# Performance work log

Hardware: AMD Instinct MI355X
Metric: run time of the kernel (lower is better)

Reference implementation:

```python
import jax, jax.numpy as jnp
import numpy as np
import math

EPS = 1e-5
NUM_HEADS = 8

def _ln(x, g, b):
    m = x.mean(-1, keepdims=True)
    v = ((x - m) ** 2).mean(-1, keepdims=True)
    return (x - m) / jnp.sqrt(v + EPS) * g + b

def _swish(x):
    return x * jax.nn.sigmoid(x)

def _rope(x):
    # lucidrains RotaryEmbedding.rotate_queries_or_keys: rotates along axis -2,
    # interleaved pair convention, base 10000.
    n, d = x.shape[-2], x.shape[-1]
    inv = 1.0 / (10000.0 ** (jnp.arange(0, d, 2, dtype=jnp.float32) / d))
    freqs = jnp.arange(n, dtype=jnp.float32)[:, None] * inv[None, :]  # (n, d/2)
    cos = jnp.repeat(jnp.cos(freqs), 2, axis=-1)  # (n, d)
    sin = jnp.repeat(jnp.sin(freqs), 2, axis=-1)
    x1, x2 = x[..., 0::2], x[..., 1::2]
    rot = jnp.stack([-x2, x1], axis=-1).reshape(x.shape)
    return x * cos + rot * sin

def _ffn(x, w1, b1, w2, b2):
    # FeedForwardModule: x + 0.5 * (Linear -> Swish -> Linear)
    return x + 0.5 * (_swish(x @ w1 + b1) @ w2 + b2)

def _mhsa(x, g, b, wq, bq, wk, bk, wv, bv, wo, bo):
    B, T, D = x.shape
    dh = D // NUM_HEADS
    y = _ln(x, g, b)
    q = (y @ wq + bq).reshape(B, T, NUM_HEADS, dh)                         # (b,t,h,d)
    k = (y @ wk + bk).reshape(B, T, NUM_HEADS, dh).transpose(0, 2, 1, 3)   # (b,h,t,d)
    v = (y @ wv + bv).reshape(B, T, NUM_HEADS, dh).transpose(0, 2, 1, 3)
    # Faithful to source: query is NOT permuted before rotary, so RoPE acts on
    # axis -2 which is heads for q and time for k (matches torch code exactly).
    q = _rope(q).transpose(0, 2, 1, 3)                                     # (b,h,t,d)
    k = _rope(k)
    score = jnp.einsum('bhtd,bhsd->bhts', q, k) / math.sqrt(D)             # /sqrt(d_model)
    attn = jax.nn.softmax(score, axis=-1)
    ctx = jnp.einsum('bhts,bhsd->bhtd', attn, v).transpose(0, 2, 1, 3).reshape(B, T, D)
    return x + ctx @ wo + bo

def _conv_module(x, g, b, pw1_w, pw1_b, dw_w, dw_b, bn_g, bn_b, pw2_w, pw2_b):
    C = dw_w.shape[-1]  # 2*dim
    y = _ln(x, g, b)
    y = jnp.einsum('btd,ed->bte', y, pw1_w) + pw1_b            # pointwise conv (b,t,4*dim)
    a, gate = y[..., :C], y[..., C:]
    y = a * jax.nn.sigmoid(gate)                                # GLU over channel dim
    y = jax.lax.conv_general_dilated(
        y, dw_w, window_strides=(1,), padding='SAME',
        dimension_numbers=('NWC', 'WIO', 'NWC'), feature_group_count=C) + dw_b
    m = y.mean(axis=(0, 1))                                     # BatchNorm1d, training stats
    v = ((y - m) ** 2).mean(axis=(0, 1))
    y = (y - m) / jnp.sqrt(v + EPS) * bn_g + bn_b
    y = _swish(y)
    y = jnp.einsum('btc,dc->btd', y, pw2_w) + pw2_b             # pointwise conv back to dim
    return x + y

def setup_inputs():
    key = jax.random.key(0)
    B, T, D, K = 8, 1024, 512, 31
    HID = 2 * D
    C = 2 * D
    ks = jax.random.split(key, 16)
    rn = lambda k, shp: jax.random.normal(k, shp, jnp.float32) * 0.02
    zeros = lambda n: jnp.zeros((n,), jnp.float32)
    ones = lambda n: jnp.ones((n,), jnp.float32)
    return dict(
        x=jax.random.normal(ks[0], (B, T, D), jnp.float32),
        ffn1_w1=rn(ks[1], (D, HID)), ffn1_b1=zeros(HID),
        ffn1_w2=rn(ks[2], (HID, D)), ffn1_b2=zeros(D),
        ln_attn_g=ones(D), ln_attn_b=zeros(D),
        wq=rn(ks[3], (D, D)), bq=zeros(D),
        wk=rn(ks[4], (D, D)), bk=zeros(D),
        wv=rn(ks[5], (D, D)), bv=zeros(D),
        wo=rn(ks[6], (D, D)), bo=zeros(D),
        conv_ln_g=ones(D), conv_ln_b=zeros(D),
        pw1_w=rn(ks[7], (2 * C, D)), pw1_b=zeros(2 * C),
        dw_w=rn(ks[8], (K, 1, C)), dw_b=zeros(C),
        bn_g=ones(C), bn_b=zeros(C),
        pw2_w=rn(ks[9], (D, C)), pw2_b=zeros(D),
        ffn2_w1=rn(ks[10], (D, HID)), ffn2_b1=zeros(HID),
        ffn2_w2=rn(ks[11], (HID, D)), ffn2_b2=zeros(D),
        ln_out_g=ones(D), ln_out_b=zeros(D),
    )

def reference(x, ffn1_w1, ffn1_b1, ffn1_w2, ffn1_b2, ln_attn_g, ln_attn_b,
              wq, bq, wk, bk, wv, bv, wo, bo,
              conv_ln_g, conv_ln_b, pw1_w, pw1_b, dw_w, dw_b, bn_g, bn_b, pw2_w, pw2_b,
              ffn2_w1, ffn2_b1, ffn2_w2, ffn2_b2, ln_out_g, ln_out_b):
    y = _ffn(x, ffn1_w1, ffn1_b1, ffn1_w2, ffn1_b2)
    y = _mhsa(y, ln_attn_g, ln_attn_b, wq, bq, wk, bk, wv, bv, wo, bo)
    y = _conv_module(y, conv_ln_g, conv_ln_b, pw1_w, pw1_b, dw_w, dw_b, bn_g, bn_b, pw2_w, pw2_b)
    y = _ffn(y, ffn2_w1, ffn2_b1, ffn2_w2, ffn2_b2)
    return _ln(y, ln_out_g, ln_out_b)
```

## Files before the change

kernel.cpp:

```cpp
#include <hip/hip_runtime.h>
#include <hip/hip_bf16.h>


#define M_ROWS 8192

using bf16x8 = __attribute__((ext_vector_type(8))) short;
using f32x4  = __attribute__((ext_vector_type(4))) float;
using s8v    = __attribute__((ext_vector_type(8))) short;
using s4v    = __attribute__((ext_vector_type(4))) short;

__device__ __forceinline__ float sigmoid_(float v) { return 1.f / (1.f + expf(-v)); }

__device__ __forceinline__ float bf2f(short s) {
  return __uint_as_float(((unsigned)(unsigned short)s) << 16);
}
__device__ __forceinline__ short f2bf(float f) {
  __hip_bfloat16 h = __float2bfloat16(f);
  return *reinterpret_cast<short*>(&h);
}

__device__ __forceinline__ void gl16(const void* g, void* l) {
  __builtin_amdgcn_global_load_lds((const __attribute__((address_space(1))) void*)g,
                                   (__attribute__((address_space(3))) void*)l, 16, 0, 0);
}

template <int BM, int BN, int BK, int EPI>
__global__ __launch_bounds__(256) void mgemm(
    const short* __restrict__ A, const short* __restrict__ Bt,
    const float* __restrict__ bias, const float* __restrict__ res,
    const short* __restrict__ resb, short* __restrict__ outb, int M, int N, int K) {
  constexpr int WR = BM / 64;
  constexpr int WC = 4 / WR;
  constexpr int NF = BN / (16 * WC);
  constexpr int KH = BK / 32;
  constexpr int APASS = (BM * BK) / 2048;
  constexpr int BPASS = (BN * BK) / 2048;
  constexpr int RPP = 2048 / BK;
  constexpr int LPS = APASS + BPASS;
  __shared__ __align__(16) short As[2][BM * BK];
  __shared__ __align__(16) short Bs[2][BN * BK];
  __shared__ __align__(16) short vstg[EPI == 4 ? 64 * 132 : 1];
  const int tid = threadIdx.x;
  const int lane = tid & 63, wid = tid >> 6;
  const int wr = wid / WC, wc = wid % WC;
  const int nbx = gridDim.x;
  const int nwg = nbx * gridDim.y;
  int id = blockIdx.y * nbx + blockIdx.x;
  id = (id & 7) * (nwg >> 3) + (id >> 3);
  const int bm = (id / nbx) * BM;
  const int bn = (id % nbx) * BN;
  f32x4 acc[4][NF];
#pragma unroll
  for (int m = 0; m < 4; ++m)
#pragma unroll
    for (int n = 0; n < NF; ++n) acc[m][n] = (f32x4){0.f, 0.f, 0.f, 0.f};
  const short* Ablk = A + (size_t)bm * K;
  const short* Bblk = Bt + (size_t)bn * K;
  const int jl = tid & (BK / 8 - 1);
  const int r0 = tid / (BK / 8);
  const int ks = ((BK == 64) ? (jl ^ (r0 & 7)) : jl) << 3;
#define STAGE(buf, k0)                                                                 \
  do {                                                                                 \
    _Pragma("unroll")                                                                  \
    for (int p = 0; p < APASS; ++p)                                                    \
      gl16(Ablk + (size_t)(r0 + p * RPP) * K + (k0) + ks,                              \
           (char*)As[buf] + p * 4096 + wid * 1024);                                    \
    _Pragma("unroll")                                                                  \
    for (int p = 0; p < BPASS; ++p)                                                    \
      gl16(Bblk + (size_t)(r0 + p * RPP) * K + (k0) + ks,                              \
           (char*)Bs[buf] + p * 4096 + wid * 1024);                                    \
  } while (0)

  STAGE(0, 0);
  STAGE(1, BK);
  const int NS = K / BK;
  const int fr = lane & 15, fg = lane >> 4;
  const int arow = wr * 64 + fr;
  const int brow = wc * (BN / WC) + fr;
  for (int i = 0; i < NS; ++i) {
    if (i + 1 < NS) {
      if constexpr (LPS == 4)      asm volatile("s_waitcnt vmcnt(4)" ::: "memory");
      else if constexpr (LPS == 3) asm volatile("s_waitcnt vmcnt(3)" ::: "memory");
      else                         asm volatile("s_waitcnt vmcnt(2)" ::: "memory");
    } else {
      asm volatile("s_waitcnt vmcnt(0)" ::: "memory");
    }
    __builtin_amdgcn_s_barrier();
    asm volatile("" ::: "memory");
    const int cur = i & 1;
    bf16x8 af[KH][4], bfr[KH][NF];
#pragma unroll
    for (int kk = 0; kk < KH; ++kk) {
      const int cx = (BK == 64) ? (((((kk << 2) + fg)) ^ (fr & 7)) << 3)
                                : ((fg << 3) + kk * 32);
#pragma unroll
      for (int m = 0; m < 4; ++m)
        af[kk][m] = *reinterpret_cast<const bf16x8*>(&As[cur][(arow + m * 16) * BK + cx]);
#pragma unroll
      for (int n = 0; n < NF; ++n)
        bfr[kk][n] = *reinterpret_cast<const bf16x8*>(&Bs[cur][(brow + n * 16) * BK + cx]);
    }
    asm volatile("s_waitcnt lgkmcnt(0)" ::: "memory");
    __builtin_amdgcn_s_barrier();
    if ((i + 2) * BK < K) STAGE(cur, (i + 2) * BK);
#pragma unroll
    for (int kk = 0; kk < KH; ++kk)
#pragma unroll
      for (int m = 0; m < 4; ++m)
#pragma unroll
        for (int n = 0; n < NF; ++n)
          acc[m][n] = __builtin_amdgcn_mfma_f32_16x16x32_bf16(af[kk][m], bfr[kk][n],
                                                              acc[m][n], 0, 0, 0);
  }
#undef STAGE
  const int orow0 = bm + wr * 64 + ((lane >> 4) << 2);
  const int ocol0 = bn + wc * (BN / WC) + fr;

  if constexpr (EPI == 4) {
    const int sel = bn >> 9;
    const float2* tbl = (const float2*)res;
    if (sel == 2) {
      const int b_ = bm >> 10, t0v = bm & 1023;
      const int hb = (bn & 511) >> 6;
#pragma unroll
      for (int pass = 0; pass < 2; ++pass) {
        __syncthreads();
        if (wc == pass) {
#pragma unroll
          for (int m = 0; m < 4; ++m) {
            const int rl = wr * 64 + ((lane >> 4) << 2) + m * 16;
#pragma unroll
            for (int n = 0; n < NF; ++n) {
              const int dl = fr + n * 16;
              const float bv = bias[bn + wc * 64 + dl];
#pragma unroll
              for (int r = 0; r < 4; ++r)
                vstg[dl * 132 + rl + r] = f2bf(acc[m][n][r] + bv);
            }
          }
        }
        __syncthreads();
#pragma unroll
        for (int it = 0; it < 4; ++it) {
          const int c = tid + (it << 8);
          const int d = c >> 4, t8 = (c & 15) << 3;
          const s8v val = *reinterpret_cast<const s8v*>(&vstg[d * 132 + t8]);
          *reinterpret_cast<s8v*>(
              &outb[(size_t)8388608 + (((size_t)((b_ << 3) + hb + pass)) << 16) +
                    ((size_t)d << 10) + t0v + t8]) = val;
        }
      }
    } else {
      const float qsc = (sel == 0) ? 0.04419417382415922f : 1.f;
#pragma unroll
      for (int n = 0; n < NF; ++n) {
        const int col = ocol0 + n * 16;
        const int h = (col >> 6) & 7, d = col & 63;
        const int p = d >> 1;
        const float bv = bias[col];
#pragma unroll
        for (int m = 0; m < 4; ++m) {
#pragma unroll
          for (int r = 0; r < 4; ++r) {
            const int row = orow0 + m * 16 + r;
            const int b_ = row >> 10, t_ = row & 1023;
            const int pos = (sel == 0) ? h : t_;
            const float2 cs = tbl[pos * 32 + p];
            float vv = acc[m][n][r] + bv;
            const float pv = __shfl_xor(vv, 1);
            float o = ((lane & 1) == 0) ? (vv * cs.x - pv * cs.y) : (vv * cs.x + pv * cs.y);
            outb[(size_t)sel * 4194304 + (((size_t)((b_ << 3) + h)) << 16) + ((size_t)t_ << 6) + d] =
                f2bf(o * qsc);
          }
        }
      }
    }
  } else if constexpr (EPI == 6) {
    const int j = bn >> 7;
#pragma unroll
    for (int m = 0; m < 4; ++m) {
#pragma unroll
      for (int np = 0; np < NF / 2; ++np) {
        const int gc = (j << 6) + ((wc * 2 + np) << 4) + fr;
        const float ba = bias[gc];
        const float bg = bias[1024 + gc];
#pragma unroll
        for (int r = 0; r < 4; ++r) {
          const int row = orow0 + m * 16 + r;
          const float a = acc[m][2 * np][r] + ba;
          const float g = acc[m][2 * np + 1][r] + bg;
          outb[(size_t)row * 1024 + gc] = f2bf(a * sigmoid_(g));
        }
      }
    }
  } else {
#pragma unroll
    for (int m = 0; m < 4; ++m) {
#pragma unroll
      for (int n = 0; n < NF; ++n) {
        const int col = ocol0 + n * 16;
        const float bv = bias[col];
#pragma unroll
        for (int r = 0; r < 4; ++r) {
          const int row = orow0 + m * 16 + r;
          float v = acc[m][n][r] + bv;
          if constexpr (EPI == 1) {
            v = v * sigmoid_(v);
          } else if constexpr (EPI == 2) {
            v += bf2f(resb[(size_t)row * N + col]);
          } else if constexpr (EPI == 3) {
            v = bf2f(resb[(size_t)row * N + col]) + 0.5f * v;
          }
          outb[(size_t)row * N + col] = f2bf(v);
        }
      }
    }
  }
}

__device__ __forceinline__ void dev_cast8(const float* in, short* out, int i) {
  const float4 a = *reinterpret_cast<const float4*>(&in[(size_t)i * 8]);
  const float4 b = *reinterpret_cast<const float4*>(&in[(size_t)i * 8 + 4]);
  s8v o = { f2bf(a.x), f2bf(a.y), f2bf(a.z), f2bf(a.w),
            f2bf(b.x), f2bf(b.y), f2bf(b.z), f2bf(b.w) };
  *reinterpret_cast<s8v*>(&out[(size_t)i * 8]) = o;
}

__global__ __launch_bounds__(256) void prep_kernel(
    const float* __restrict__ x, short* __restrict__ xb,
    const float* __restrict__ f1w1, short* __restrict__ wf1w1,
    const float* __restrict__ f1w2, short* __restrict__ wf1w2,
    const float* __restrict__ wq, const float* __restrict__ wk,
    const float* __restrict__ wv, short* __restrict__ wqkv,
    const float* __restrict__ wo, short* __restrict__ wwo,
    const float* __restrict__ pw1, short* __restrict__ wpw1,
    const float* __restrict__ pw2, short* __restrict__ wpw2,
    const float* __restrict__ f2w1, short* __restrict__ wf2w1,
    const float* __restrict__ f2w2, short* __restrict__ wf2w2,
    const float* __restrict__ bq, const float* __restrict__ bk,
    const float* __restrict__ bv, float* __restrict__ bqkv,
    float* __restrict__ rtbl) {
  __shared__ float t[32][33];
  const int blk = blockIdx.x, tid = threadIdx.x;
  const float* tin = nullptr;
  short* tout = nullptr;
  int tK = 0, tN = 0, tr = 0, tnbx = 0;
  if (blk < 2048) {
    dev_cast8(x, xb, blk * 256 + tid);
    return;
  } else if (blk < 2560) { tin = f1w1; tout = wf1w1; tK = 512; tN = 1024; tr = blk - 2048; tnbx = 32; }
  else if (blk < 3072)   { tin = f1w2; tout = wf1w2; tK = 1024; tN = 512; tr = blk - 2560; tnbx = 16; }
  else if (blk < 3328)   { tin = wq; tout = wqkv; tK = 512; tN = 512; tr = blk - 3072; tnbx = 16; }
  else if (blk < 3584)   { tin = wk; tout = wqkv + 512 * 512; tK = 512; tN = 512; tr = blk - 3328; tnbx = 16; }
  else if (blk < 3840)   { tin = wv; tout = wqkv + 1024 * 512; tK = 512; tN = 512; tr = blk - 3584; tnbx = 16; }
  else if (blk < 4096)   { tin = wo; tout = wwo; tK = 512; tN = 512; tr = blk - 3840; tnbx = 16; }
  else if (blk < 4608) {
    const int idx = (blk - 4096) * 256 + tid;
    const int pc = idx >> 6, kk = (idx & 63) << 3;
    const int j = pc >> 7, s = (pc >> 4) & 7, fr = pc & 15;
    const int oc = ((s & 1) << 10) + (j << 6) + ((s >> 1) << 4) + fr;
    const float4 a = *reinterpret_cast<const float4*>(&pw1[(size_t)oc * 512 + kk]);
    const float4 b = *reinterpret_cast<const float4*>(&pw1[(size_t)oc * 512 + kk + 4]);
    s8v o = { f2bf(a.x), f2bf(a.y), f2bf(a.z), f2bf(a.w),
              f2bf(b.x), f2bf(b.y), f2bf(b.z), f2bf(b.w) };
    *reinterpret_cast<s8v*>(&wpw1[(size_t)pc * 512 + kk]) = o;
    return;
  } else if (blk < 4864) {
    dev_cast8(pw2, wpw2, (blk - 4608) * 256 + tid);
    return;
  } else if (blk < 5376) { tin = f2w1; tout = wf2w1; tK = 512; tN = 1024; tr = blk - 4864; tnbx = 32; }
  else if (blk < 5888)   { tin = f2w2; tout = wf2w2; tK = 1024; tN = 512; tr = blk - 5376; tnbx = 16; }
  else if (blk < 6016) {
    const int i = (blk - 5888) * 256 + tid;
    const int tt = i >> 5, p = i & 31;
    const float inv = exp2f(-(float)p * 0.41524101186092f);
    float s, c;
    sincosf((float)tt * inv, &s, &c);
    rtbl[i * 2] = c;
    rtbl[i * 2 + 1] = s;
    return;
  } else {
    const int i = (blk - 6016) * 256 + tid;
    if (i < 1536) bqkv[i] = i < 512 ? bq[i] : (i < 1024 ? bk[i - 512] : bv[i - 1024]);
    return;
  }
  const int n0 = (tr % tnbx) << 5, k0 = (tr / tnbx) << 5;
  const int tx = tid & 31, ty = tid >> 5;
  for (int r = ty; r < 32; r += 8) t[r][tx] = tin[(size_t)(k0 + r) * tN + n0 + tx];
  __syncthreads();
  for (int r = ty; r < 32; r += 8) tout[(size_t)(n0 + r) * tK + k0 + tx] = f2bf(t[tx][r]);
}

template <typename OT>
__global__ __launch_bounds__(256) void ln_kernel(
    const short* __restrict__ in, const float* __restrict__ g,
    const float* __restrict__ b, OT* __restrict__ out) {
  __shared__ float sm[4];
  const size_t row = blockIdx.x;
  const int tid = threadIdx.x;
  const short* x = in + (row << 9);
  const int pr = *reinterpret_cast<const int*>(&x[tid << 1]);
  const float v0 = bf2f((short)(pr & 0xffff));
  const float v1 = bf2f((short)(((unsigned)pr) >> 16));
  float s = v0 + v1;
  for (int o = 32; o; o >>= 1) s += __shfl_xor(s, o);
  if ((tid & 63) == 0) sm[tid >> 6] = s;
  __syncthreads();
  const float mean = (sm[0] + sm[1] + sm[2] + sm[3]) * (1.f / 512.f);
  __syncthreads();
  const float d0 = v0 - mean, d1 = v1 - mean;
  float q = d0 * d0 + d1 * d1;
  for (int o = 32; o; o >>= 1) q += __shfl_xor(q, o);
  if ((tid & 63) == 0) sm[tid >> 6] = q;
  __syncthreads();
  const float var = (sm[0] + sm[1] + sm[2] + sm[3]) * (1.f / 512.f);
  const float inv = rsqrtf(var + 1e-5f);
  const float2 gv = *reinterpret_cast<const float2*>(&g[tid << 1]);
  const float2 bv = *reinterpret_cast<const float2*>(&b[tid << 1]);
  const float o0 = d0 * inv * gv.x + bv.x;
  const float o1 = d1 * inv * gv.y + bv.y;
  if constexpr (sizeof(OT) == 2) {
    const int pk = (int)(unsigned short)f2bf(o0) | ((int)(unsigned short)f2bf(o1) << 16);
    *reinterpret_cast<int*>(&out[(row << 9) + (tid << 1)]) = pk;
  } else {
    float2 o = {o0, o1};
    *reinterpret_cast<float2*>(&out[(row << 9) + (tid << 1)]) = o;
  }
}

__global__ __launch_bounds__(256) void attn_mfma_kernel(
    const short* __restrict__ q, const short* __restrict__ k,
    const short* __restrict__ vt, short* __restrict__ ctx) {
  __shared__ __align__(16) short Ks[64][72];
  __shared__ __align__(16) short VsT[64][72];
  __shared__ __align__(16) short Ps[2][64][72];
  const int bx = ((blockIdx.x & 7) << 6) | (blockIdx.x >> 3);
  const int bh = bx >> 3, qt = bx & 7;
  const int b_ = bh >> 3, h_ = bh & 7;
  const int tid = threadIdx.x, lane = tid & 63, w = tid >> 6;
  const int t0 = qt << 7;
  const short* qbase = q + ((size_t)bh << 16) + ((size_t)t0 << 6);
  const short* kbase = k + ((size_t)bh << 16);
  const short* vtbase = vt + ((size_t)bh << 16);
  const int sr = tid >> 2, scg = (tid & 3) << 4;
  short* Qtmp = &Ps[0][0][0];
  {
    const int sr2 = tid >> 1, sc2 = (tid & 1) << 5;
#pragma unroll
    for (int j = 0; j < 4; ++j) {
      const s8v v = *reinterpret_cast<const s8v*>(&qbase[(size_t)sr2 * 64 + sc2 + j * 8]);
      *reinterpret_cast<s8v*>(&Qtmp[sr2 * 72 + sc2 + j * 8]) = v;
    }
    const s8v k0a = *reinterpret_cast<const s8v*>(&kbase[(size_t)sr * 64 + scg]);
    const s8v k0b = *reinterpret_cast<const s8v*>(&kbase[(size_t)sr * 64 + scg + 8]);
    *reinterpret_cast<s8v*>(&Ks[sr][scg]) = k0a;
    *reinterpret_cast<s8v*>(&Ks[sr][scg + 8]) = k0b;
    const s8v v0a = *reinterpret_cast<const s8v*>(&vtbase[((size_t)sr << 10) + scg]);
    const s8v v0b = *reinterpret_cast<const s8v*>(&vtbase[((size_t)sr << 10) + scg + 8]);
    *reinterpret_cast<s8v*>(&VsT[sr][scg]) = v0a;
    *reinterpret_cast<s8v*>(&VsT[sr][scg + 8]) = v0b;
  }
  __syncthreads();
  const int fr = lane & 15, fg = lane >> 4;
  const int koff0 = fg << 3;
  bf16x8 qf[2][2];
#pragma unroll
  for (int a = 0; a < 2; ++a) {
    qf[a][0] = *reinterpret_cast<const bf16x8*>(&Qtmp[(a * 64 + w * 16 + fr) * 72 + koff0]);
    qf[a][1] = *reinterpret_cast<const bf16x8*>(&Qtmp[(a * 64 + w * 16 + fr) * 72 + 32 + koff0]);
  }
  __syncthreads();
  float m[2][4], l[2][4];
  f32x4 outv[2][4];
#pragma unroll
  for (int a = 0; a < 2; ++a)
#pragma unroll
    for (int r = 0; r < 4; ++r) { m[a][r] = -1e30f; l[a][r] = 0.f; }
#pragma unroll
  for (int a = 0; a < 2; ++a)
#pragma unroll
    for (int n = 0; n < 4; ++n) outv[a][n] = (f32x4){0.f, 0.f, 0.f, 0.f};

  for (int i = 0; i < 16; ++i) {
    s8v nk0, nk1, nv0, nv1;
    const bool pf = (i < 15);
    if (pf) {
      const int kn = (i + 1) << 6;
      nk0 = *reinterpret_cast<const s8v*>(&kbase[(size_t)(kn + sr) * 64 + scg]);
      nk1 = *reinterpret_cast<const s8v*>(&kbase[(size_t)(kn + sr) * 64 + scg + 8]);
      nv0 = *reinterpret_cast<const s8v*>(&vtbase[((size_t)sr << 10) + kn + scg]);
      nv1 = *reinterpret_cast<const s8v*>(&vtbase[((size_t)sr << 10) + kn + scg + 8]);
    }
    f32x4 sacc[2][4];
    __builtin_amdgcn_s_setprio(1);
#pragma unroll
    for (int n = 0; n < 4; ++n) {
      const bf16x8 kf0 = *reinterpret_cast<const bf16x8*>(&Ks[n * 16 + fr][koff0]);
      const bf16x8 kf1 = *reinterpret_cast<const bf16x8*>(&Ks[n * 16 + fr][32 + koff0]);
#pragma unroll
      for (int a = 0; a < 2; ++a) {
        sacc[a][n] = (f32x4){0.f, 0.f, 0.f, 0.f};
        sacc[a][n] = __builtin_amdgcn_mfma_f32_16x16x32_bf16(qf[a][0], kf0, sacc[a][n], 0, 0, 0);
        sacc[a][n] = __builtin_amdgcn_mfma_f32_16x16x32_bf16(qf[a][1], kf1, sacc[a][n], 0, 0, 0);
      }
    }
    __builtin_amdgcn_s_setprio(0);
    float vm[2][4];
    bool ok = true;
#pragma unroll
    for (int a = 0; a < 2; ++a)
#pragma unroll
      for (int r = 0; r < 4; ++r) {
        vm[a][r] = fmaxf(fmaxf(sacc[a][0][r], sacc[a][1][r]),
                         fmaxf(sacc[a][2][r], sacc[a][3][r]));
        ok = ok && (vm[a][r] <= m[a][r] + 8.f);
      }
    if (__all(ok)) {
#pragma unroll
      for (int a = 0; a < 2; ++a)
#pragma unroll
        for (int r = 0; r < 4; ++r) {
          const float p0 = __expf(sacc[a][0][r] - m[a][r]), p1 = __expf(sacc[a][1][r] - m[a][r]);
          const float p2 = __expf(sacc[a][2][r] - m[a][r]), p3 = __expf(sacc[a][3][r] - m[a][r]);
          l[a][r] += p0 + p1 + p2 + p3;
          const int qr = w * 16 + (fg << 2) + r;
          Ps[a][qr][fr] = f2bf(p0);
          Ps[a][qr][16 + fr] = f2bf(p1);
          Ps[a][qr][32 + fr] = f2bf(p2);
          Ps[a][qr][48 + fr] = f2bf(p3);
        }
    } else {
#pragma unroll
      for (int a = 0; a < 2; ++a)
#pragma unroll
        for (int r = 0; r < 4; ++r) {
          float rm = vm[a][r];
          rm = fmaxf(rm, __shfl_xor(rm, 1));
          rm = fmaxf(rm, __shfl_xor(rm, 2));
          rm = fmaxf(rm, __shfl_xor(rm, 4));
          rm = fmaxf(rm, __shfl_xor(rm, 8));
          const float nm = fmaxf(m[a][r], rm);
          const float al = __expf(m[a][r] - nm);
          m[a][r] = nm;
          const float p0 = __expf(sacc[a][0][r] - nm), p1 = __expf(sacc[a][1][r] - nm);
          const float p2 = __expf(sacc[a][2][r] - nm), p3 = __expf(sacc[a][3][r] - nm);
          l[a][r] = l[a][r] * al + (p0 + p1 + p2 + p3);
          outv[a][0][r] *= al; outv[a][1][r] *= al;
          outv[a][2][r] *= al; outv[a][3][r] *= al;
          const int qr = w * 16 + (fg << 2) + r;
          Ps[a][qr][fr] = f2bf(p0);
          Ps[a][qr][16 + fr] = f2bf(p1);
          Ps[a][qr][32 + fr] = f2bf(p2);
          Ps[a][qr][48 + fr] = f2bf(p3);
        }
    }
    __syncthreads();
    if (pf) {
      *reinterpret_cast<s8v*>(&Ks[sr][scg]) = nk0;
      *reinterpret_cast<s8v*>(&Ks[sr][scg + 8]) = nk1;
    }
    __builtin_amdgcn_s_setprio(1);
#pragma unroll
    for (int a = 0; a < 2; ++a) {
      const bf16x8 pa0 = *reinterpret_cast<const bf16x8*>(&Ps[a][w * 16 + fr][koff0]);
      const bf16x8 pa1 = *reinterpret_cast<const bf16x8*>(&Ps[a][w * 16 + fr][32 + koff0]);
#pragma unroll
      for (int n = 0; n < 4; ++n) {
        const bf16x8 vf0 = *reinterpret_cast<const bf16x8*>(&VsT[n * 16 + fr][koff0]);
        const bf16x8 vf1 = *reinterpret_cast<const bf16x8*>(&VsT[n * 16 + fr][32 + koff0]);
        outv[a][n] = __builtin_amdgcn_mfma_f32_16x16x32_bf16(pa0, vf0, outv[a][n], 0, 0, 0);
        outv[a][n] = __builtin_amdgcn_mfma_f32_16x16x32_bf16(pa1, vf1, outv[a][n], 0, 0, 0);
      }
    }
    __builtin_amdgcn_s_setprio(0);
    __syncthreads();
    if (pf) {
      *reinterpret_cast<s8v*>(&VsT[sr][scg]) = nv0;
      *reinterpret_cast<s8v*>(&VsT[sr][scg + 8]) = nv1;
    }
  }
#pragma unroll
  for (int a = 0; a < 2; ++a)
#pragma unroll
    for (int r = 0; r < 4; ++r) {
      float L = l[a][r];
      L += __shfl_xor(L, 1);
      L += __shfl_xor(L, 2);
      L += __shfl_xor(L, 4);
      L += __shfl_xor(L, 8);
      const float inv = 1.f / L;
      const int t = t0 + a * 64 + w * 16 + (fg << 2) + r;
      const size_t base = (((size_t)((b_ << 10) | t)) << 9) + (h_ << 6);
#pragma unroll
      for (int n = 0; n < 4; ++n)
        ctx[base + n * 16 + fr] = f2bf(outv[a][n][r] * inv);
    }
}

__global__ __launch_bounds__(256) void dwconv_kernel(
    const short* __restrict__ in, const float* __restrict__ w,
    const float* __restrict__ bias, short* __restrict__ out) {
  __shared__ __align__(16) short tile[286 * 72];
  __shared__ float wlds[31 * 64];
  const int id = blockIdx.x;
  const int ct = id & 15, tt = (id >> 4) & 3;
  const size_t b = id >> 6;
  const int c0 = ct << 6, t0 = tt << 8;
  const int tid = threadIdx.x;
  for (int i = tid; i < 31 * 64; i += 256) {
    const int kk = i >> 6, c = i & 63;
    wlds[i] = w[kk * 1024 + c0 + c];
  }
  for (int i = tid; i < 286 * 8; i += 256) {
    const int row = i >> 3, seg = i & 7;
    const int gt = t0 - 15 + row;
    s8v val = {};
    if (gt >= 0 && gt < 1024)
      val = *reinterpret_cast<const s8v*>(&in[(b << 20) + ((size_t)gt << 10) + c0 + (seg << 3)]);
    *reinterpret_cast<s8v*>(&tile[row * 72 + (seg << 3)]) = val;
  }
  __syncthreads();
  const int cg = tid & 7, tg = tid >> 3;
  const int tl = tg << 3;
  float acc[8][8];
  const float4 b0 = *reinterpret_cast<const float4*>(&bias[c0 + (cg << 3)]);
  const float4 b1 = *reinterpret_cast<const float4*>(&bias[c0 + (cg << 3) + 4]);
#pragma unroll
  for (int t = 0; t < 8; ++t) {
    acc[t][0] = b0.x; acc[t][1] = b0.y; acc[t][2] = b0.z; acc[t][3] = b0.w;
    acc[t][4] = b1.x; acc[t][5] = b1.y; acc[t][6] = b1.z; acc[t][7] = b1.w;
  }
  for (int kk = 0; kk < 31; ++kk) {
    const float4 w0 = *reinterpret_cast<const float4*>(&wlds[kk * 64 + (cg << 3)]);
    const float4 w1 = *reinterpret_cast<const float4*>(&wlds[kk * 64 + (cg << 3) + 4]);
#pragma unroll
    for (int t = 0; t < 8; ++t) {
      const s8v xv = *reinterpret_cast<const s8v*>(&tile[(tl + t + kk) * 72 + (cg << 3)]);
      acc[t][0] = fmaf(bf2f(xv[0]), w0.x, acc[t][0]);
      acc[t][1] = fmaf(bf2f(xv[1]), w0.y, acc[t][1]);
      acc[t][2] = fmaf(bf2f(xv[2]), w0.z, acc[t][2]);
      acc[t][3] = fmaf(bf2f(xv[3]), w0.w, acc[t][3]);
      acc[t][4] = fmaf(bf2f(xv[4]), w1.x, acc[t][4]);
      acc[t][5] = fmaf(bf2f(xv[5]), w1.y, acc[t][5]);
      acc[t][6] = fmaf(bf2f(xv[6]), w1.z, acc[t][6]);
      acc[t][7] = fmaf(bf2f(xv[7]), w1.w, acc[t][7]);
    }
  }
#pragma unroll
  for (int t = 0; t < 8; ++t) {
    s8v o;
#pragma unroll
    for (int j = 0; j < 8; ++j) o[j] = f2bf(acc[t][j]);
    *reinterpret_cast<s8v*>(&out[(b << 20) + ((size_t)(t0 + tl + t) << 10) + c0 + (cg << 3)]) = o;
  }
}

__global__ __launch_bounds__(256) void bn_stats_kernel(
    const short* __restrict__ y, float* __restrict__ ps, float* __restrict__ pq) {
  const int tid = threadIdx.x;
  const int c4 = tid << 2;
  const size_t r0 = (size_t)blockIdx.x * 32;
  float s[4] = {0, 0, 0, 0}, q[4] = {0, 0, 0, 0};
  for (int r = 0; r < 32; ++r) {
    const s4v v = *reinterpret_cast<const s4v*>(&y[((r0 + r) << 10) + c4]);
#pragma unroll
    for (int j = 0; j < 4; ++j) {
      const float f = bf2f(v[j]);
      s[j] += f;
      q[j] = fmaf(f, f, q[j]);
    }
  }
#pragma unroll
  for (int j = 0; j < 4; ++j) {
    ps[(size_t)blockIdx.x * 1024 + c4 + j] = s[j];
    pq[(size_t)blockIdx.x * 1024 + c4 + j] = q[j];
  }
}

__global__ __launch_bounds__(256) void bn_finalize_kernel(
    const float* __restrict__ ps, const float* __restrict__ pq, float* __restrict__ stats) {
  const int c = blockIdx.x * 256 + threadIdx.x;
  float s = 0.f, q = 0.f;
  for (int i = 0; i < 256; ++i) {
    s += ps[i * 1024 + c];
    q += pq[i * 1024 + c];
  }
  const float mean = s * (1.f / 8192.f);
  const float var = q * (1.f / 8192.f) - mean * mean;
  stats[c] = mean;
  stats[1024 + c] = rsqrtf(fmaxf(var, 0.f) + 1e-5f);
}

__global__ __launch_bounds__(256) void bn_apply_kernel(
    const short* __restrict__ y, const float* __restrict__ g, const float* __restrict__ b,
    const float* __restrict__ stats, short* __restrict__ out) {
  const size_t i = (size_t)blockIdx.x * 256 + threadIdx.x;
  const size_t f = i << 2;
  const int c = (int)(f & 1023);
  const s4v yv = *reinterpret_cast<const s4v*>(&y[f]);
  s4v o;
#pragma unroll
  for (int j = 0; j < 4; ++j) {
    const float v = (bf2f(yv[j]) - stats[c + j]) * stats[1024 + c + j] * g[c + j] + b[c + j];
    o[j] = f2bf(v * sigmoid_(v));
  }
  *reinterpret_cast<s4v*>(&out[f]) = o;
}

extern "C" void kernel_launch(void* const* d_in, const int* in_sizes, int n_in,
                              void* d_out, int out_size, void* d_ws, size_t ws_size,
                              hipStream_t stream) {
  const float* x        = (const float*)d_in[0];
  const float* ffn1_w1  = (const float*)d_in[1];
  const float* ffn1_b1  = (const float*)d_in[2];
  const float* ffn1_w2  = (const float*)d_in[3];
  const float* ffn1_b2  = (const float*)d_in[4];
  const float* ln_att_g = (const float*)d_in[5];
  const float* ln_att_b = (const float*)d_in[6];
  const float* wq       = (const float*)d_in[7];
  const float* bq       = (const float*)d_in[8];
  const float* wk       = (const float*)d_in[9];
  const float* bk       = (const float*)d_in[10];
  const float* wv       = (const float*)d_in[11];
  const float* bv       = (const float*)d_in[12];
  const float* wo_      = (const float*)d_in[13];
  const float* bo       = (const float*)d_in[14];
  const float* cln_g    = (const float*)d_in[15];
  const float* cln_b    = (const float*)d_in[16];
  const float* pw1_w    = (const float*)d_in[17];
  const float* pw1_b    = (const float*)d_in[18];
  const float* dw_w     = (const float*)d_in[19];
  const float* dw_b     = (const float*)d_in[20];
  const float* bn_g     = (const float*)d_in[21];
  const float* bn_b     = (const float*)d_in[22];
  const float* pw2_w    = (const float*)d_in[23];
  const float* pw2_b    = (const float*)d_in[24];
  const float* ffn2_w1  = (const float*)d_in[25];
  const float* ffn2_b1  = (const float*)d_in[26];
  const float* ffn2_w2  = (const float*)d_in[27];
  const float* ffn2_b2  = (const float*)d_in[28];
  const float* ln_out_g = (const float*)d_in[29];
  const float* ln_out_b = (const float*)d_in[30];

  char* wsb = (char*)d_ws;
  const size_t MB = 1u << 20;
  short* buf_y = (short*)(wsb);
  char* Bre = wsb + 16 * MB;
  short* qkv16 = (short*)(Bre);
  short* lnq  = (short*)(Bre + 48 * MB);
  short* ctx  = (short*)(Bre + 56 * MB);
  short* h1   = (short*)(Bre);
  short* xb   = (short*)(Bre + 16 * MB);
  short* gluo = (short*)(Bre);
  short* bno  = (short*)(Bre + 48 * MB);
  char* Cre = wsb + 80 * MB;
  short* lnc  = (short*)(Cre);
  short* dwo16= (short*)(Cre + 8 * MB);
  char* Dre = wsb + 112 * MB;
  short* w_f1w1 = (short*)(Dre);
  short* w_f1w2 = (short*)(Dre + 1 * MB);
  short* w_qkv  = (short*)(Dre + 2 * MB);
  short* w_wo   = (short*)(Dre + 3 * MB + 512 * 1024);
  short* w_pw1  = (short*)(Dre + 4 * MB);
  short* w_pw2  = (short*)(Dre + 6 * MB);
  short* w_f2w1 = (short*)(Dre + 7 * MB);
  short* w_f2w2 = (short*)(Dre + 8 * MB);
  float* bqkv   = (float*)(Dre + 9 * MB);
  float* ps     = (float*)(Dre + 9 * MB + 8192);
  float* pq     = (float*)(Dre + 10 * MB + 8192);
  float* stats  = (float*)(Dre + 11 * MB + 8192);
  float* rtbl   = (float*)(Dre + 12 * MB);

  const dim3 blk(256);

  prep_kernel<<<6022, blk, 0, stream>>>(
      x, xb, ffn1_w1, w_f1w1, ffn1_w2, w_f1w2, wq, wk, wv, w_qkv, wo_, w_wo,
      pw1_w, w_pw1, pw2_w, w_pw2, ffn2_w1, w_f2w1, ffn2_w2, w_f2w2,
      bq, bk, bv, bqkv, rtbl);

  mgemm<64, 64, 64, 1><<<dim3(16, 128), blk, 0, stream>>>(xb, w_f1w1, ffn1_b1, nullptr, nullptr, h1, M_ROWS, 1024, 512);
  mgemm<64, 64, 64, 3><<<dim3(8, 128), blk, 0, stream>>>(h1, w_f1w2, ffn1_b2, nullptr, xb, buf_y, M_ROWS, 512, 1024);

  ln_kernel<short><<<M_ROWS, blk, 0, stream>>>(buf_y, ln_att_g, ln_att_b, lnq);
  mgemm<128, 128, 32, 4><<<dim3(12, 64), blk, 0, stream>>>(lnq, w_qkv, bqkv, rtbl, nullptr, qkv16, M_ROWS, 1536, 512);
  attn_mfma_kernel<<<512, blk, 0, stream>>>(qkv16, qkv16 + 4194304, qkv16 + 8388608, ctx);
  mgemm<64, 64, 64, 2><<<dim3(8, 128), blk, 0, stream>>>(ctx, w_wo, bo, nullptr, buf_y, buf_y, M_ROWS, 512, 512);

  ln_kernel<short><<<M_ROWS, blk, 0, stream>>>(buf_y, cln_g, cln_b, lnc);
  mgemm<128, 128, 32, 6><<<dim3(16, 64), blk, 0, stream>>>(lnc, w_pw1, pw1_b, nullptr, nullptr, gluo, M_ROWS, 2048, 512);
  dwconv_kernel<<<512, blk, 0, stream>>>(gluo, dw_w, dw_b, dwo16);
  bn_stats_kernel<<<256, blk, 0, stream>>>(dwo16, ps, pq);
  bn_finalize_kernel<<<4, blk, 0, stream>>>(ps, pq, stats);
  bn_apply_kernel<<<8192, blk, 0, stream>>>(dwo16, bn_g, bn_b, stats, bno);
  mgemm<64, 64, 64, 2><<<dim3(8, 128), blk, 0, stream>>>(bno, w_pw2, pw2_b, nullptr, buf_y, buf_y, M_ROWS, 512, 1024);

  mgemm<64, 64, 64, 1><<<dim3(16, 128), blk, 0, stream>>>(buf_y, w_f2w1, ffn2_b1, nullptr, nullptr, h1, M_ROWS, 1024, 512);
  mgemm<64, 64, 64, 3><<<dim3(8, 128), blk, 0, stream>>>(h1, w_f2w2, ffn2_b2, nullptr, buf_y, buf_y, M_ROWS, 512, 1024);

  ln_kernel<float><<<M_ROWS, blk, 0, stream>>>(buf_y, ln_out_g, ln_out_b, (float*)d_out);
}
```

Before: 284.4 us.

## Fuse BN statistics into depthwise conv and widen small GEMM tiles

Per-channel batch-norm partial sums and sums of squares are now computed inside the depthwise conv kernel from its fp32 accumulators and reduced through shared memory. This removes the separate bn_stats pass over the conv output, and the finalize kernel reduces over 32 partials instead of 256. The 64x64 GEMM launches switch to 64x128 tiles with half as many blocks, which gives more reuse per block but fewer blocks to fill the device. A vmcnt(6) wait case is added for the 6-load-per-stage configuration. Statistics now come from fp32 values before bf16 rounding, a slight numeric difference.

```diff
diff --git a/kernel.cpp b/kernel.cpp
--- a/kernel.cpp
+++ b/kernel.cpp
@@ -79,7 +79,8 @@
   const int brow = wc * (BN / WC) + fr;
   for (int i = 0; i < NS; ++i) {
     if (i + 1 < NS) {
-      if constexpr (LPS == 4)      asm volatile("s_waitcnt vmcnt(4)" ::: "memory");
+      if constexpr (LPS == 6)      asm volatile("s_waitcnt vmcnt(6)" ::: "memory");
+      else if constexpr (LPS == 4) asm volatile("s_waitcnt vmcnt(4)" ::: "memory");
       else if constexpr (LPS == 3) asm volatile("s_waitcnt vmcnt(3)" ::: "memory");
       else                         asm volatile("s_waitcnt vmcnt(2)" ::: "memory");
     } else {
@@ -499,7 +500,8 @@
 
 __global__ __launch_bounds__(256) void dwconv_kernel(
     const short* __restrict__ in, const float* __restrict__ w,
-    const float* __restrict__ bias, short* __restrict__ out) {
+    const float* __restrict__ bias, short* __restrict__ out,
+    float* __restrict__ ps, float* __restrict__ pq) {
   __shared__ __align__(16) short tile[286 * 72];
   __shared__ float wlds[31 * 64];
   const int id = blockIdx.x;
@@ -553,27 +555,37 @@
     for (int j = 0; j < 8; ++j) o[j] = f2bf(acc[t][j]);
     *reinterpret_cast<s8v*>(&out[(b << 20) + ((size_t)(t0 + tl + t) << 10) + c0 + (cg << 3)]) = o;
   }
-}
-
-__global__ __launch_bounds__(256) void bn_stats_kernel(
-    const short* __restrict__ y, float* __restrict__ ps, float* __restrict__ pq) {
-  const int tid = threadIdx.x;
-  const int c4 = tid << 2;
-  const size_t r0 = (size_t)blockIdx.x * 32;
-  float s[4] = {0, 0, 0, 0}, q[4] = {0, 0, 0, 0};
-  for (int r = 0; r < 32; ++r) {
-    const s4v v = *reinterpret_cast<const s4v*>(&y[((r0 + r) << 10) + c4]);
-#pragma unroll
-    for (int j = 0; j < 4; ++j) {
-      const float f = bf2f(v[j]);
-      s[j] += f;
-      q[j] = fmaf(f, f, q[j]);
-    }
-  }
-#pragma unroll
-  for (int j = 0; j < 4; ++j) {
-    ps[(size_t)blockIdx.x * 1024 + c4 + j] = s[j];
-    pq[(size_t)blockIdx.x * 1024 + c4 + j] = q[j];
+  float s8_[8], q8_[8];
+#pragma unroll
+  for (int j = 0; j < 8; ++j) {
+    float S = 0.f, Q = 0.f;
+#pragma unroll
+    for (int t = 0; t < 8; ++t) {
+      S += acc[t][j];
+      Q = fmaf(acc[t][j], acc[t][j], Q);
+    }
+    s8_[j] = S;
+    q8_[j] = Q;
+  }
+  __syncthreads();
+  float* fred = (float*)tile;
+#pragma unroll
+  for (int j = 0; j < 8; ++j) {
+    fred[tid * 16 + j] = s8_[j];
+    fred[tid * 16 + 8 + j] = q8_[j];
+  }
+  __syncthreads();
+  if (tid < 64) {
+    const int cg_ = tid >> 3, j_ = tid & 7;
+    float S = 0.f, Q = 0.f;
+    for (int tg_ = 0; tg_ < 32; ++tg_) {
+      const int th = tg_ * 8 + cg_;
+      S += fred[th * 16 + j_];
+      Q += fred[th * 16 + 8 + j_];
+    }
+    const int pidx = ((int)b << 2) + tt;
+    ps[pidx * 1024 + c0 + tid] = S;
+    pq[pidx * 1024 + c0 + tid] = Q;
   }
 }
 
@@ -581,7 +593,7 @@
     const float* __restrict__ ps, const float* __restrict__ pq, float* __restrict__ stats) {
   const int c = blockIdx.x * 256 + threadIdx.x;
   float s = 0.f, q = 0.f;
-  for (int i = 0; i < 256; ++i) {
+  for (int i = 0; i < 32; ++i) {
     s += ps[i * 1024 + c];
     q += pq[i * 1024 + c];
   }
@@ -678,24 +690,23 @@
       pw1_w, w_pw1, pw2_w, w_pw2, ffn2_w1, w_f2w1, ffn2_w2, w_f2w2,
       bq, bk, bv, bqkv, rtbl);
 
-  mgemm<64, 64, 64, 1><<<dim3(16, 128), blk, 0, stream>>>(xb, w_f1w1, ffn1_b1, nullptr, nullptr, h1, M_ROWS, 1024, 512);
-  mgemm<64, 64, 64, 3><<<dim3(8, 128), blk, 0, stream>>>(h1, w_f1w2, ffn1_b2, nullptr, xb, buf_y, M_ROWS, 512, 1024);
+  mgemm<64, 128, 64, 1><<<dim3(8, 128), blk, 0, stream>>>(xb, w_f1w1, ffn1_b1, nullptr, nullptr, h1, M_ROWS, 1024, 512);
+  mgemm<64, 128, 64, 3><<<dim3(4, 128), blk, 0, stream>>>(h1, w_f1w2, ffn1_b2, nullptr, xb, buf_y, M_ROWS, 512, 1024);
 
   ln_kernel<short><<<M_ROWS, blk, 0, stream>>>(buf_y, ln_att_g, ln_att_b, lnq);
   mgemm<128, 128, 32, 4><<<dim3(12, 64), blk, 0, stream>>>(lnq, w_qkv, bqkv, rtbl, nullptr, qkv16, M_ROWS, 1536, 512);
   attn_mfma_kernel<<<512, blk, 0, stream>>>(qkv16, qkv16 + 4194304, qkv16 + 8388608, ctx);
-  mgemm<64, 64, 64, 2><<<dim3(8, 128), blk, 0, stream>>>(ctx, w_wo, bo, nullptr, buf_y, buf_y, M_ROWS, 512, 512);
+  mgemm<64, 128, 64, 2><<<dim3(4, 128), blk, 0, stream>>>(ctx, w_wo, bo, nullptr, buf_y, buf_y, M_ROWS, 512, 512);
 
   ln_kernel<short><<<M_ROWS, blk, 0, stream>>>(buf_y, cln_g, cln_b, lnc);
   mgemm<128, 128, 32, 6><<<dim3(16, 64), blk, 0, stream>>>(lnc, w_pw1, pw1_b, nullptr, nullptr, gluo, M_ROWS, 2048, 512);
-  dwconv_kernel<<<512, blk, 0, stream>>>(gluo, dw_w, dw_b, dwo16);
-  bn_stats_kernel<<<256, blk, 0, stream>>>(dwo16, ps, pq);
+  dwconv_kernel<<<512, blk, 0, stream>>>(gluo, dw_w, dw_b, dwo16, ps, pq);
   bn_finalize_kernel<<<4, blk, 0, stream>>>(ps, pq, stats);
   bn_apply_kernel<<<8192, blk, 0, stream>>>(dwo16, bn_g, bn_b, stats, bno);
-  mgemm<64, 64, 64, 2><<<dim3(8, 128), blk, 0, stream>>>(bno, w_pw2, pw2_b, nullptr, buf_y, buf_y, M_ROWS, 512, 1024);
-
-  mgemm<64, 64, 64, 1><<<dim3(16, 128), blk, 0, stream>>>(buf_y, w_f2w1, ffn2_b1, nullptr, nullptr, h1, M_ROWS, 1024, 512);
-  mgemm<64, 64, 64, 3><<<dim3(8, 128), blk, 0, stream>>>(h1, w_f2w2, ffn2_b2, nullptr, buf_y, buf_y, M_ROWS, 512, 1024);
+  mgemm<64, 128, 64, 2><<<dim3(4, 128), blk, 0, stream>>>(bno, w_pw2, pw2_b, nullptr, buf_y, buf_y, M_ROWS, 512, 1024);
+
+  mgemm<64, 128, 64, 1><<<dim3(8, 128), blk, 0, stream>>>(buf_y, w_f2w1, ffn2_b1, nullptr, nullptr, h1, M_ROWS, 1024, 512);
+  mgemm<64, 128, 64, 3><<<dim3(4, 128), blk, 0, stream>>>(h1, w_f2w2, ffn2_b2, nullptr, buf_y, buf_y, M_ROWS, 512, 1024);
 
   ln_kernel<float><<<M_ROWS, blk, 0, stream>>>(buf_y, ln_out_g, ln_out_b, (float*)d_out);
 }
```

New measurement: 261.7 us. 1.09x faster.
